# Kernel optimization log

Hardware: AMD Instinct MI355X
Metric: run time of the kernel (lower is better)

The kernel has to match this reference:

```python
import jax, jax.numpy as jnp
import numpy as np

B, S, D = 2, 4096, 2048
H = 16
DN, DR = 128, 64          # qk_nope_head_dim, qk_rope_head_dim
DQK = DN + DR             # 192
DV = 128                  # v_head_dim
QL, KVL = 512, 512        # q_lora_rank, kv_lora_rank
L = 64                    # block_len
SCALE = DQK ** -0.5
ROPE_THETA = 10000.0


def rms_norm(x, w, eps=1e-6):
    x = x.astype(jnp.float32)
    return x * jax.lax.rsqrt(jnp.mean(x * x, axis=-1, keepdims=True) + eps) * w


def apply_rope(x, cos, sin):
    # x: [b, s, h, d]; cos/sin: [s, d//2]; pairs are consecutive (view(-1,2))
    shp = x.shape
    x2 = x.reshape(shp[:-1] + (-1, 2))
    xr, xi = x2[..., 0], x2[..., 1]
    c = cos[None, :, None, :]
    s_ = sin[None, :, None, :]
    yr = xr * c - xi * s_
    yi = xr * s_ + xi * c
    return jnp.stack([yr, yi], axis=-1).reshape(shp)


def ssa(q, k, v, init_state):
    # chunked causal linear attention; q,k: [b,s,h,dk], v: [b,s,h,dv]
    b, s, h, dk = q.shape
    dv = v.shape[-1]
    nc = s // L
    qc = q.reshape(b, nc, L, h, dk)
    kc = k.reshape(b, nc, L, h, dk)
    vc = v.reshape(b, nc, L, h, dv)
    # per-chunk k^T v outer products -> [b,c,h,dk,dv]
    kv = jnp.einsum('bclhk,bclhv->bchkv', kc, vc)
    cs = jnp.cumsum(kv, axis=1)
    # exclusive prefix (state at chunk start) + initial state
    states = jnp.concatenate([jnp.zeros_like(cs[:, :1]), cs[:, :-1]], axis=1) + init_state[:, None]
    inter = jnp.einsum('bclhk,bchkv->bclhv', qc, states)
    sc = jnp.einsum('bclhk,bcmhk->bchlm', qc, kc)
    mask = jnp.tril(jnp.ones((L, L), dtype=bool))
    sc = jnp.where(mask, sc, 0.0)
    intra = jnp.einsum('bchlm,bcmhv->bclhv', sc, vc)
    return (inter + intra).reshape(b, s, h, dv)


def setup_inputs() -> dict:
    key = jax.random.key(0)
    ks = jax.random.split(key, 8)
    x = jax.random.normal(ks[0], (B, S, D), dtype=jnp.float32)
    # rope tables for qk_rope_head_dim
    inv = 1.0 / (ROPE_THETA ** (np.arange(0, DR, 2, dtype=np.float32) / DR))
    ang = np.outer(np.arange(S, dtype=np.float32), inv)
    cos = jnp.asarray(np.cos(ang), dtype=jnp.float32)
    sin = jnp.asarray(np.sin(ang), dtype=jnp.float32)
    std = 0.02
    wq_a = jax.random.normal(ks[1], (QL, D), dtype=jnp.float32) * std
    wq_b = jax.random.normal(ks[2], (H * DQK, QL), dtype=jnp.float32) * std
    wkv_a = jax.random.normal(ks[3], (KVL + DR, D), dtype=jnp.float32) * std
    wkv_b = jax.random.normal(ks[4], (H * (DN + DV), KVL), dtype=jnp.float32) * std
    wo = jax.random.normal(ks[5], (D, H * DV), dtype=jnp.float32) * std
    q_norm_w = jnp.ones((QL,), dtype=jnp.float32)
    kv_norm_w = jnp.ones((KVL,), dtype=jnp.float32)
    init_state = jnp.zeros((B, H, DQK, DV), dtype=jnp.float32)
    return {"x": x, "start_pos": 0, "cos": cos, "sin": sin,
            "wq_a": wq_a, "wq_b": wq_b, "wkv_a": wkv_a, "wkv_b": wkv_b,
            "wo": wo, "q_norm_w": q_norm_w, "kv_norm_w": kv_norm_w,
            "init_state": init_state}


def reference(x, start_pos, cos, sin, wq_a, wq_b, wkv_a, wkv_b, wo,
              q_norm_w, kv_norm_w, init_state):
    b, s, _ = x.shape
    q = rms_norm(x @ wq_a.T, q_norm_w) @ wq_b.T
    q = q.reshape(b, s, H, DQK)
    q_nope, q_pe = q[..., :DN], q[..., DN:]
    q_pe = apply_rope(q_pe, cos, sin)
    kvp = x @ wkv_a.T
    kv_lat, k_pe = kvp[..., :KVL], kvp[..., KVL:]
    k_pe = apply_rope(k_pe[:, :, None, :], cos, sin)  # [b,s,1,DR]
    kv = rms_norm(kv_lat, kv_norm_w) @ wkv_b.T
    kv = kv.reshape(b, s, H, DN + DV)
    k_nope, v = kv[..., :DN], kv[..., DN:]
    q = jnp.concatenate([q_nope, q_pe], axis=-1)
    k = jnp.concatenate([k_nope, jnp.broadcast_to(k_pe, (b, s, H, DR))], axis=-1)
    q = jax.nn.elu(q) + 1.0
    k = jax.nn.elu(k) + 1.0
    out = ssa(q, k, v, init_state) * SCALE
    out = out.reshape(b, s, H * DV) @ wo.T
    return out
```

## Files before the change

### kernel.cpp

```cpp
#include <hip/hip_runtime.h>

static __device__ __align__(256) unsigned char g_ws[645200000];

typedef __attribute__((ext_vector_type(8))) __bf16 bf16x8;
typedef __attribute__((ext_vector_type(4))) float  f32x4;
typedef __attribute__((ext_vector_type(8))) unsigned short u16x8;

__device__ __forceinline__ short f2bf(float f) {
    union { float f; unsigned u; } v; v.f = f;
    unsigned r = v.u + 0x7FFFu + ((v.u >> 16) & 1u);
    return (short)(r >> 16);
}
__device__ __forceinline__ float bf2f(unsigned short u) {
    union { unsigned u; float f; } v; v.u = ((unsigned)u) << 16;
    return v.f;
}
__device__ __forceinline__ float elu1(float x) {
    return x > 0.f ? x + 1.f : __expf(x);
}
__device__ __forceinline__ void gload_lds16(const void* g, void* l) {
    __builtin_amdgcn_global_load_lds(
        (const __attribute__((address_space(1))) unsigned int*)g,
        (__attribute__((address_space(3))) unsigned int*)l, 16, 0, 0);
}

#define MFMA16(a, b, c) __builtin_amdgcn_mfma_f32_16x16x32_bf16((a), (b), (c), 0, 0, 0)

__global__ __launch_bounds__(256) void cvt_bf16(
    const float* __restrict__ src, short* __restrict__ dst, int n)
{
    const int i = (blockIdx.x * 256 + threadIdx.x) * 4;
    if (i < n) {
        const float4 v = *(const float4*)(src + i);
        ushort4 o;
        o.x = (unsigned short)f2bf(v.x);
        o.y = (unsigned short)f2bf(v.y);
        o.z = (unsigned short)f2bf(v.z);
        o.w = (unsigned short)f2bf(v.w);
        *(ushort4*)(dst + i) = o;
    }
}

template <int OUT_BF16>
__global__ __launch_bounds__(512, 2) void gemm256(
    const short* __restrict__ A, int lda,
    const short* __restrict__ Bt, int ldb,
    void* __restrict__ Cv, int ldc,
    int Nvalid, int K, int nbx)
{
    __shared__ short lds[65536];
    char* ldsB = (char*)lds;
    const int t = threadIdx.x;
    const int lane = t & 63, w = t >> 6;

    const int cpx = gridDim.x >> 3;
    const int id = (blockIdx.x & 7) * cpx + (blockIdx.x >> 3);
    const int row0 = (id % nbx) * 256;
    const int col0 = (id / nbx) * 256;

    const int r_in = lane >> 2;
    const int sw_src = ((lane & 3) << 4) ^ (((lane >> 4) & 3) << 4);
    const char* aSrc = (const char*)A + ((size_t)(row0 + w * 32 + r_in) * lda) * 2 + sw_src;
    const char* bSrc = (const char*)Bt + ((size_t)(col0 + w * 32 + r_in) * ldb) * 2 + sw_src;
    const size_t aStep = (size_t)lda * 32;
    const size_t bStep = (size_t)ldb * 32;
    char* aDst = ldsB + (w * 2) * 1024 + lane * 16;
    char* bDst = ldsB + 65536 + (w * 2) * 1024 + lane * 16;

    const int wr = (w >> 2) * 128, wc = (w & 3) * 64;
    const int l15 = lane & 15;
    const int kxor = ((lane >> 4) * 16) ^ (((l15 >> 2) & 3) << 4);

    const int NT = K >> 5;

    auto STAGE = [&](int j) {
        const int sb = (j & 3) * 16384;
        const size_t kb = (size_t)j * 64;
        gload_lds16(aSrc + kb,         aDst + sb);
        gload_lds16(aSrc + kb + aStep, aDst + sb + 1024);
        gload_lds16(bSrc + kb,         bDst + sb);
        gload_lds16(bSrc + kb + bStep, bDst + sb + 1024);
    };

    f32x4 acc[8][4];
#pragma unroll
    for (int i = 0; i < 8; ++i)
#pragma unroll
        for (int j = 0; j < 4; ++j) acc[i][j] = (f32x4){0.f, 0.f, 0.f, 0.f};

    STAGE(0); STAGE(1); STAGE(2);

#pragma unroll 1
    for (int kt = 0; kt < NT; ++kt) {
        if (kt < NT - 2)        asm volatile("s_waitcnt vmcnt(8)" ::: "memory");
        else if (kt == NT - 2)  asm volatile("s_waitcnt vmcnt(4)" ::: "memory");
        else                    asm volatile("s_waitcnt vmcnt(0)" ::: "memory");
        __builtin_amdgcn_s_barrier();
        __builtin_amdgcn_sched_barrier(0);
        if (kt + 3 < NT) STAGE(kt + 3);
        const char* aS = ldsB + (kt & 3) * 16384;
        const char* bS = ldsB + 65536 + (kt & 3) * 16384;
        bf16x8 af[8], bf4[4];
#pragma unroll
        for (int i = 0; i < 8; ++i)
            af[i] = *(const bf16x8*)(aS + (wr + i * 16 + l15) * 64 + kxor);
#pragma unroll
        for (int j = 0; j < 4; ++j)
            bf4[j] = *(const bf16x8*)(bS + (wc + j * 16 + l15) * 64 + kxor);
        __builtin_amdgcn_s_setprio(1);
#pragma unroll
        for (int i = 0; i < 8; ++i)
#pragma unroll
            for (int j = 0; j < 4; ++j)
                acc[i][j] = MFMA16(af[i], bf4[j], acc[i][j]);
        __builtin_amdgcn_s_setprio(0);
    }

    const int rbase = (lane >> 4) * 4;
#pragma unroll
    for (int i = 0; i < 8; ++i)
#pragma unroll
        for (int j = 0; j < 4; ++j) {
            const int cc = col0 + wc + j * 16 + l15;
            if (cc < Nvalid) {
#pragma unroll
                for (int q = 0; q < 4; ++q) {
                    const size_t o = (size_t)(row0 + wr + i * 16 + rbase + q) * ldc + cc;
                    if (OUT_BF16) ((short*)Cv)[o] = f2bf(acc[i][j][q]);
                    else          ((float*)Cv)[o] = acc[i][j][q];
                }
            }
        }
}

__global__ __launch_bounds__(256) void rms_rope(
    const short* __restrict__ Y1,
    const float* __restrict__ qw, const float* __restrict__ kvw,
    const float* __restrict__ cosT, const float* __restrict__ sinT,
    short* __restrict__ qn, short* __restrict__ kvn, float* __restrict__ kpe)
{
    __shared__ float red[256];
    const int row = blockIdx.x;
    const int s = row & 4095;
    const int t = threadIdx.x;
    const unsigned short* yr = (const unsigned short*)(Y1 + (size_t)row * 1088);

    float v0 = bf2f(yr[t]), v1 = bf2f(yr[t + 256]);
    red[t] = v0 * v0 + v1 * v1;
    __syncthreads();
    for (int off = 128; off > 0; off >>= 1) {
        if (t < off) red[t] += red[t + off];
        __syncthreads();
    }
    float rs = rsqrtf(red[0] / 512.f + 1e-6f);
    __syncthreads();
    qn[(size_t)row * 512 + t]       = f2bf(v0 * rs * qw[t]);
    qn[(size_t)row * 512 + t + 256] = f2bf(v1 * rs * qw[t + 256]);

    float u0 = bf2f(yr[512 + t]), u1 = bf2f(yr[768 + t]);
    red[t] = u0 * u0 + u1 * u1;
    __syncthreads();
    for (int off = 128; off > 0; off >>= 1) {
        if (t < off) red[t] += red[t + off];
        __syncthreads();
    }
    float rs2 = rsqrtf(red[0] / 512.f + 1e-6f);
    kvn[(size_t)row * 512 + t]       = f2bf(u0 * rs2 * kvw[t]);
    kvn[(size_t)row * 512 + t + 256] = f2bf(u1 * rs2 * kvw[t + 256]);

    if (t < 32) {
        float xr = bf2f(yr[1024 + 2 * t]), xi = bf2f(yr[1024 + 2 * t + 1]);
        float cc = cosT[(size_t)s * 32 + t], sn = sinT[(size_t)s * 32 + t];
        kpe[(size_t)row * 64 + 2 * t]     = xr * cc - xi * sn;
        kpe[(size_t)row * 64 + 2 * t + 1] = xr * sn + xi * cc;
    }
}

__global__ __launch_bounds__(192) void build_q(
    const short* __restrict__ qbig,
    const float* __restrict__ cosT, const float* __restrict__ sinT,
    short* __restrict__ q_ssa)
{
    const int row = blockIdx.x;
    const int s = row & 4095;
    const int b = row >> 12;
    const int d = threadIdx.x;
    const unsigned short* qr = (const unsigned short*)(qbig + (size_t)row * 3072);
#pragma unroll 1
    for (int h = 0; h < 16; ++h) {
        float val;
        if (d < 128) {
            val = bf2f(qr[h * 192 + d]);
        } else {
            const int p = (d - 128) >> 1;
            const float xr = bf2f(qr[h * 192 + 128 + 2 * p]);
            const float xi = bf2f(qr[h * 192 + 128 + 2 * p + 1]);
            const float cc = cosT[(size_t)s * 32 + p];
            const float sn = sinT[(size_t)s * 32 + p];
            val = ((d & 1) == 0) ? (xr * cc - xi * sn) : (xr * sn + xi * cc);
        }
        val = elu1(val);
        q_ssa[((size_t)(b * 16 + h) * 4096 + s) * 192 + d] = f2bf(val);
    }
}

__global__ __launch_bounds__(256) void build_kv(
    const short* __restrict__ kvbig, const float* __restrict__ kpe,
    short* __restrict__ k_ssa, short* __restrict__ v_ssa)
{
    const int row = blockIdx.x;
    const int s = row & 4095;
    const int b = row >> 12;
    const int t = threadIdx.x;
    const unsigned short* kr = (const unsigned short*)(kvbig + (size_t)row * 4096);
    const float* pe = kpe + (size_t)row * 64;
#pragma unroll 1
    for (int h = 0; h < 16; ++h) {
        const size_t kbase = ((size_t)(b * 16 + h) * 4096 + s) * 192;
        const size_t vbase = ((size_t)(b * 16 + h) * 4096 + s) * 128;
        if (t < 128) {
            k_ssa[kbase + t] = f2bf(elu1(bf2f(kr[h * 256 + t])));
            v_ssa[vbase + t] = (short)kr[h * 256 + 128 + t];
        } else if (t < 192) {
            const int d = t - 128;
            k_ssa[kbase + 128 + d] = f2bf(elu1(pe[d]));
        }
    }
}

__global__ __launch_bounds__(256) void init_t_kern(
    const float* __restrict__ init, float* __restrict__ initT)
{
    __shared__ float tile[32][33];
    const int bh = blockIdx.y;
    const int tk = blockIdx.x % 6, tv = blockIdx.x / 6;
    const int r0 = threadIdx.x >> 5, c = threadIdx.x & 31;
    const float* src = init + (size_t)bh * 24576;
    float* dst = initT + (size_t)bh * 24576;
#pragma unroll
    for (int p = 0; p < 4; ++p) {
        const int rr = r0 + 8 * p;
        tile[rr][c] = src[(size_t)(tk * 32 + rr) * 128 + tv * 32 + c];
    }
    __syncthreads();
#pragma unroll
    for (int p = 0; p < 4; ++p) {
        const int rr = r0 + 8 * p;
        dst[(size_t)(tv * 32 + rr) * 192 + tk * 32 + c] = tile[c][rr];
    }
}

__global__ __launch_bounds__(256, 3) void ssa_kv(
    const short* __restrict__ k_ssa, const short* __restrict__ v_ssa,
    short* __restrict__ kvcT)
{
    __shared__ short smem[25600];
    short (*lkt)[72] = (short(*)[72])smem;
    short (*lvt)[72] = (short(*)[72])(smem + 192 * 72);
    short (*outT)[200] = (short(*)[200])smem;
    const int c = blockIdx.x, h = blockIdx.y, b = blockIdx.z;
    const int bh = b * 16 + h;
    const short* Kc = k_ssa + ((size_t)bh * 4096 + c * 64) * 192;
    const short* Vc = v_ssa + ((size_t)bh * 4096 + c * 64) * 128;
    const int t = threadIdx.x, lane = t & 63, w = t >> 6;
    const int l15 = lane & 15, kg = (lane >> 4) * 8, rbase = (lane >> 4) * 4;

    for (int i = t; i < 64 * 48; i += 256) {
        const int row = i / 48, c4 = (i % 48) * 4;
        ushort4 kv4 = *(const ushort4*)(Kc + (size_t)row * 192 + c4);
        lkt[c4 + 0][row] = (short)kv4.x;
        lkt[c4 + 1][row] = (short)kv4.y;
        lkt[c4 + 2][row] = (short)kv4.z;
        lkt[c4 + 3][row] = (short)kv4.w;
    }
    for (int i = t; i < 64 * 32; i += 256) {
        const int row = i >> 5, c4 = (i & 31) * 4;
        ushort4 vv = *(const ushort4*)(Vc + (size_t)row * 128 + c4);
        lvt[c4 + 0][row] = (short)vv.x;
        lvt[c4 + 1][row] = (short)vv.y;
        lvt[c4 + 2][row] = (short)vv.z;
        lvt[c4 + 3][row] = (short)vv.w;
    }
    __syncthreads();

    f32x4 acc[2][12];
#pragma unroll
    for (int i = 0; i < 2; ++i)
#pragma unroll
        for (int j = 0; j < 12; ++j) acc[i][j] = (f32x4){0.f, 0.f, 0.f, 0.f};
#pragma unroll
    for (int ks = 0; ks < 2; ++ks) {
        bf16x8 af[2];
#pragma unroll
        for (int i = 0; i < 2; ++i) af[i] = *(const bf16x8*)&lvt[w * 32 + i * 16 + l15][ks * 32 + kg];
#pragma unroll
        for (int j = 0; j < 12; ++j) {
            const bf16x8 bk = *(const bf16x8*)&lkt[j * 16 + l15][ks * 32 + kg];
#pragma unroll
            for (int i = 0; i < 2; ++i) acc[i][j] = MFMA16(af[i], bk, acc[i][j]);
        }
    }
    __syncthreads();
#pragma unroll
    for (int i = 0; i < 2; ++i)
#pragma unroll
        for (int j = 0; j < 12; ++j)
#pragma unroll
            for (int q = 0; q < 4; ++q)
                outT[w * 32 + i * 16 + rbase + q][j * 16 + l15] = f2bf(acc[i][j][q]);
    __syncthreads();

    short* kvp = kvcT + ((size_t)bh * 64 + c) * 24576;
    for (int i = t; i < 3072; i += 256) {
        const int s8 = i * 8;
        const int row = s8 / 192, col = s8 % 192;
        *(u16x8*)(kvp + s8) = *(const u16x8*)&outT[row][col];
    }
}

__global__ __launch_bounds__(256) void ssa_scan(
    short* __restrict__ kvc, const float* __restrict__ initT)
{
    const int bh = blockIdx.y;
    const int e8 = (blockIdx.x * 256 + threadIdx.x) * 8;
    float st[8];
    {
        const float4 i0 = *(const float4*)(initT + (size_t)bh * 24576 + e8);
        const float4 i1 = *(const float4*)(initT + (size_t)bh * 24576 + e8 + 4);
        st[0] = i0.x; st[1] = i0.y; st[2] = i0.z; st[3] = i0.w;
        st[4] = i1.x; st[5] = i1.y; st[6] = i1.z; st[7] = i1.w;
    }
    short* p = kvc + (size_t)bh * 64 * 24576 + e8;
    for (int cc = 0; cc < 64; ++cc) {
        const u16x8 v = *(const u16x8*)p;
        u16x8 o;
#pragma unroll
        for (int j = 0; j < 8; ++j) o[j] = (unsigned short)f2bf(st[j]);
        *(u16x8*)p = o;
#pragma unroll
        for (int j = 0; j < 8; ++j) st[j] += bf2f(v[j]);
        p += 24576;
    }
}

__global__ __launch_bounds__(256, 2) void ssa_out(
    const short* __restrict__ q_ssa, const short* __restrict__ k_ssa,
    const short* __restrict__ v_ssa, const short* __restrict__ states,
    short* __restrict__ attnb)
{
    __shared__ short lk[64][200];
    __shared__ short lvt[128][72];
    __shared__ short lst[128][104];
    __shared__ short lsc[64][72];
    const int c = blockIdx.x, h = blockIdx.y, b = blockIdx.z;
    const int bh = b * 16 + h;
    const short* Qb = q_ssa + ((size_t)bh * 4096 + c * 64) * 192;
    const short* Kc = k_ssa + ((size_t)bh * 4096 + c * 64) * 192;
    const short* Vc = v_ssa + ((size_t)bh * 4096 + c * 64) * 128;
    const short* st = states + ((size_t)bh * 64 + c) * 24576;
    const int t = threadIdx.x, lane = t & 63, w = t >> 6;
    const int l15 = lane & 15, kg = (lane >> 4) * 8, rbase = (lane >> 4) * 4;

    bf16x8 aq[6];
    {
        const short* Qr = Qb + (size_t)(w * 16 + l15) * 192 + kg;
#pragma unroll
        for (int ks = 0; ks < 6; ++ks) aq[ks] = *(const bf16x8*)(Qr + ks * 32);
    }
    for (int i = t; i < 1536; i += 256) {
        const int row = i / 24, c8 = (i % 24) * 8;
        *(u16x8*)&lk[row][c8] = *(const u16x8*)(Kc + (size_t)row * 192 + c8);
    }
    for (int i = t; i < 2048; i += 256) {
        const int row = i >> 5, c4 = (i & 31) * 4;
        ushort4 vv = *(const ushort4*)(Vc + (size_t)row * 128 + c4);
        lvt[c4 + 0][row] = (short)vv.x;
        lvt[c4 + 1][row] = (short)vv.y;
        lvt[c4 + 2][row] = (short)vv.z;
        lvt[c4 + 3][row] = (short)vv.w;
    }
    for (int i = t; i < 1536; i += 256) {
        const int row = i / 12, c8 = (i % 12) * 8;
        *(u16x8*)&lst[row][c8] = *(const u16x8*)(st + (size_t)row * 192 + c8);
    }
    __syncthreads();

    {
        f32x4 sc[4];
#pragma unroll
        for (int j = 0; j < 4; ++j) sc[j] = (f32x4){0.f, 0.f, 0.f, 0.f};
#pragma unroll
        for (int ks = 0; ks < 6; ++ks)
#pragma unroll
            for (int j = 0; j < 4; ++j) {
                const bf16x8 bk = *(const bf16x8*)&lk[j * 16 + l15][ks * 32 + kg];
                sc[j] = MFMA16(aq[ks], bk, sc[j]);
            }
#pragma unroll
        for (int j = 0; j < 4; ++j)
#pragma unroll
            for (int q = 0; q < 4; ++q) {
                const int l = w * 16 + rbase + q;
                const int m = j * 16 + l15;
                lsc[l][m] = f2bf((m <= l) ? sc[j][q] : 0.f);
            }
    }
    __syncthreads();

    f32x4 acc[8];
#pragma unroll
    for (int j = 0; j < 8; ++j) acc[j] = (f32x4){0.f, 0.f, 0.f, 0.f};
#pragma unroll
    for (int ks = 0; ks < 2; ++ks) {
        const bf16x8 as = *(const bf16x8*)&lsc[w * 16 + l15][ks * 32 + kg];
#pragma unroll
        for (int j = 0; j < 8; ++j) {
            const bf16x8 bv = *(const bf16x8*)&lvt[j * 16 + l15][ks * 32 + kg];
            acc[j] = MFMA16(as, bv, acc[j]);
        }
    }
#pragma unroll
    for (int ks = 0; ks < 3; ++ks)
#pragma unroll
        for (int j = 0; j < 8; ++j) {
            const bf16x8 bs = *(const bf16x8*)&lst[j * 16 + l15][ks * 32 + kg];
            acc[j] = MFMA16(aq[ks], bs, acc[j]);
        }
    __syncthreads();
    for (int i = t; i < 1536; i += 256) {
        const int row = i / 12, c8 = (i % 12) * 8;
        *(u16x8*)&lst[row][c8] = *(const u16x8*)(st + (size_t)row * 192 + 96 + c8);
    }
    __syncthreads();
#pragma unroll
    for (int ks = 3; ks < 6; ++ks)
#pragma unroll
        for (int j = 0; j < 8; ++j) {
            const bf16x8 bs = *(const bf16x8*)&lst[j * 16 + l15][(ks - 3) * 32 + kg];
            acc[j] = MFMA16(aq[ks], bs, acc[j]);
        }

    const float scale = 0.07216878364870322f;
#pragma unroll
    for (int j = 0; j < 8; ++j)
#pragma unroll
        for (int q = 0; q < 4; ++q) {
            const int l = w * 16 + rbase + q;
            const int dv = j * 16 + l15;
            attnb[((size_t)(b * 4096 + c * 64 + l)) * 2048 + h * 128 + dv] = f2bf(acc[j][q] * scale);
        }
}

extern "C" void kernel_launch(void* const* d_in, const int* in_sizes, int n_in,
                              void* d_out, int out_size, void* d_ws, size_t ws_size,
                              hipStream_t stream) {
    const float* x     = (const float*)d_in[0];
    const float* cosT  = (const float*)d_in[2];
    const float* sinT  = (const float*)d_in[3];
    const float* wq_a  = (const float*)d_in[4];
    const float* wq_b  = (const float*)d_in[5];
    const float* wkv_a = (const float*)d_in[6];
    const float* wkv_b = (const float*)d_in[7];
    const float* wo    = (const float*)d_in[8];
    const float* qw    = (const float*)d_in[9];
    const float* kvw   = (const float*)d_in[10];
    const float* init  = (const float*)d_in[11];
    float* out = (float*)d_out;

    void* base = nullptr;
    hipGetSymbolAddress(&base, HIP_SYMBOL(g_ws));
    char* ws = (char*)base;
    size_t off = 0;
    auto take = [&](size_t bytes) -> char* {
        char* p = ws + off;
        off += (bytes + 255) & ~(size_t)255;
        return p;
    };
    short* xb    = (short*)take((size_t)8192 * 2048 * 2);
    short* wab   = (short*)take((size_t)1280 * 2048 * 2);
    short* wqbb  = (short*)take((size_t)3072 * 512 * 2);
    short* wkvbb = (short*)take((size_t)4096 * 512 * 2);
    short* wob   = (short*)take((size_t)2048 * 2048 * 2);
    short* y1b   = (short*)take((size_t)8192 * 1088 * 2);
    short* qnb   = (short*)take((size_t)8192 * 512 * 2);
    short* kvnb  = (short*)take((size_t)8192 * 512 * 2);
    float* kpe   = (float*)take((size_t)8192 * 64 * 4);
    short* qbig  = (short*)take((size_t)8192 * 3072 * 2);
    short* kvbig = (short*)take((size_t)8192 * 4096 * 2);
    short* qs    = (short*)take((size_t)2 * 16 * 4096 * 192 * 2);
    short* ksb   = (short*)take((size_t)2 * 16 * 4096 * 192 * 2);
    short* vsb   = (short*)take((size_t)2 * 16 * 4096 * 128 * 2);
    short* kvcT  = (short*)take((size_t)2048 * 24576 * 2);
    float* initT = (float*)take((size_t)32 * 24576 * 4);
    short* attnb = (short*)take((size_t)8192 * 2048 * 2);

    cvt_bf16<<<(8192 * 2048 / 4 + 255) / 256, 256, 0, stream>>>(x, xb, 8192 * 2048);
    cvt_bf16<<<(512 * 2048 / 4 + 255) / 256, 256, 0, stream>>>(wq_a, wab, 512 * 2048);
    cvt_bf16<<<(576 * 2048 / 4 + 255) / 256, 256, 0, stream>>>(wkv_a, wab + (size_t)512 * 2048, 576 * 2048);
    hipMemsetAsync(wab + (size_t)1088 * 2048, 0, (size_t)192 * 2048 * 2, stream);
    cvt_bf16<<<(3072 * 512 / 4 + 255) / 256, 256, 0, stream>>>(wq_b, wqbb, 3072 * 512);
    cvt_bf16<<<(4096 * 512 / 4 + 255) / 256, 256, 0, stream>>>(wkv_b, wkvbb, 4096 * 512);
    cvt_bf16<<<(2048 * 2048 / 4 + 255) / 256, 256, 0, stream>>>(wo, wob, 2048 * 2048);
    init_t_kern<<<dim3(24, 32), 256, 0, stream>>>(init, initT);

    gemm256<1><<<160, 512, 0, stream>>>(xb, 2048, wab, 2048, y1b, 1088, 1088, 2048, 32);
    rms_rope<<<8192, 256, 0, stream>>>(y1b, qw, kvw, cosT, sinT, qnb, kvnb, kpe);
    gemm256<1><<<384, 512, 0, stream>>>(qnb, 512, wqbb, 512, qbig, 3072, 3072, 512, 32);
    build_q<<<8192, 192, 0, stream>>>(qbig, cosT, sinT, qs);
    gemm256<1><<<512, 512, 0, stream>>>(kvnb, 512, wkvbb, 512, kvbig, 4096, 4096, 512, 32);
    build_kv<<<8192, 256, 0, stream>>>(kvbig, kpe, ksb, vsb);
    ssa_kv<<<dim3(64, 16, 2), 256, 0, stream>>>(ksb, vsb, kvcT);
    ssa_scan<<<dim3(12, 32), 256, 0, stream>>>(kvcT, initT);
    ssa_out<<<dim3(64, 16, 2), 256, 0, stream>>>(qs, ksb, vsb, kvcT, attnb);
    gemm256<0><<<256, 512, 0, stream>>>(attnb, 2048, wob, 2048, out, 2048, 2048, 2048, 32);
}
```

Baseline: 641.0 us.

## Fuse RoPE/ELU/head scatter into GEMM epilogues and switch GEMM to K=64 double buffering

Removes the build_q and build_kv kernels by moving RoPE, ELU and the per-head layout scatter into the q and kv up-projection GEMM epilogues. This eliminates the qbig/kvbig intermediate round trips through HBM. The k_pe RoPE+ELU now happens in rms_rope in bf16, and a small build_kpe kernel broadcasts it across heads. Separately, the GEMM main loop changes from a 4-stage K=32 pipeline to a 2-stage K=64 pipeline with a new XOR swizzle and an extra barrier per iteration. The trade-off is a scattered-store epilogue and possibly less latency hiding in the GEMM.

```diff
diff --git a/kernel.cpp b/kernel.cpp
--- a/kernel.cpp
+++ b/kernel.cpp
@@ -41,15 +41,15 @@
     }
 }
 
-template <int OUT_BF16>
+template <int EPI>
 __global__ __launch_bounds__(512, 2) void gemm256(
     const short* __restrict__ A, int lda,
     const short* __restrict__ Bt, int ldb,
-    void* __restrict__ Cv, int ldc,
-    int Nvalid, int K, int nbx)
-{
-    __shared__ short lds[65536];
-    char* ldsB = (char*)lds;
+    void* __restrict__ C0, void* __restrict__ C1, int ldc,
+    int Nvalid, int K, int nbx,
+    const float* __restrict__ cosT, const float* __restrict__ sinT)
+{
+    __shared__ char ldsB[131072];
     const int t = threadIdx.x;
     const int lane = t & 63, w = t >> 6;
 
@@ -58,28 +58,30 @@
     const int row0 = (id % nbx) * 256;
     const int col0 = (id / nbx) * 256;
 
-    const int r_in = lane >> 2;
-    const int sw_src = ((lane & 3) << 4) ^ (((lane >> 4) & 3) << 4);
-    const char* aSrc = (const char*)A + ((size_t)(row0 + w * 32 + r_in) * lda) * 2 + sw_src;
-    const char* bSrc = (const char*)Bt + ((size_t)(col0 + w * 32 + r_in) * ldb) * 2 + sw_src;
-    const size_t aStep = (size_t)lda * 32;
-    const size_t bStep = (size_t)ldb * 32;
-    char* aDst = ldsB + (w * 2) * 1024 + lane * 16;
-    char* bDst = ldsB + 65536 + (w * 2) * 1024 + lane * 16;
+    const int r8 = lane >> 3;
+    const int srcb = (((lane & 7) ^ r8) << 4);
+    const char* aSrc = (const char*)A + ((size_t)(row0 + w * 32 + r8) * lda) * 2 + srcb;
+    const char* bSrc = (const char*)Bt + ((size_t)(col0 + w * 32 + r8) * ldb) * 2 + srcb;
+    const size_t aRow8 = (size_t)lda * 16;
+    const size_t bRow8 = (size_t)ldb * 16;
+    char* aDst = ldsB + w * 4096 + lane * 16;
+    char* bDst = ldsB + 65536 + w * 4096 + lane * 16;
 
     const int wr = (w >> 2) * 128, wc = (w & 3) * 64;
     const int l15 = lane & 15;
-    const int kxor = ((lane >> 4) * 16) ^ (((l15 >> 2) & 3) << 4);
-
-    const int NT = K >> 5;
+    const int g16 = (lane >> 4) * 16;
+    const int rxor = (l15 & 7) << 4;
+
+    const int NT = K >> 6;
 
     auto STAGE = [&](int j) {
-        const int sb = (j & 3) * 16384;
-        const size_t kb = (size_t)j * 64;
-        gload_lds16(aSrc + kb,         aDst + sb);
-        gload_lds16(aSrc + kb + aStep, aDst + sb + 1024);
-        gload_lds16(bSrc + kb,         bDst + sb);
-        gload_lds16(bSrc + kb + bStep, bDst + sb + 1024);
+        const int sb = (j & 1) * 32768;
+        const size_t kb = (size_t)j * 128;
+#pragma unroll
+        for (int p = 0; p < 4; ++p) {
+            gload_lds16(aSrc + kb + p * aRow8, aDst + sb + p * 1024);
+            gload_lds16(bSrc + kb + p * bRow8, bDst + sb + p * 1024);
+        }
     };
 
     f32x4 acc[8][4];
@@ -88,25 +90,25 @@
 #pragma unroll
         for (int j = 0; j < 4; ++j) acc[i][j] = (f32x4){0.f, 0.f, 0.f, 0.f};
 
-    STAGE(0); STAGE(1); STAGE(2);
+    STAGE(0); STAGE(1);
 
 #pragma unroll 1
     for (int kt = 0; kt < NT; ++kt) {
-        if (kt < NT - 2)        asm volatile("s_waitcnt vmcnt(8)" ::: "memory");
-        else if (kt == NT - 2)  asm volatile("s_waitcnt vmcnt(4)" ::: "memory");
-        else                    asm volatile("s_waitcnt vmcnt(0)" ::: "memory");
+        if (kt + 1 < NT) asm volatile("s_waitcnt vmcnt(8)" ::: "memory");
+        else             asm volatile("s_waitcnt vmcnt(0)" ::: "memory");
         __builtin_amdgcn_s_barrier();
         __builtin_amdgcn_sched_barrier(0);
-        if (kt + 3 < NT) STAGE(kt + 3);
-        const char* aS = ldsB + (kt & 3) * 16384;
-        const char* bS = ldsB + 65536 + (kt & 3) * 16384;
+        const char* aS = ldsB + (kt & 1) * 32768;
+        const char* bS = ldsB + 65536 + (kt & 1) * 32768;
         bf16x8 af[8], bf4[4];
 #pragma unroll
         for (int i = 0; i < 8; ++i)
-            af[i] = *(const bf16x8*)(aS + (wr + i * 16 + l15) * 64 + kxor);
+            af[i] = *(const bf16x8*)(aS + (wr + i * 16 + l15) * 128 + (g16 ^ rxor));
 #pragma unroll
         for (int j = 0; j < 4; ++j)
-            bf4[j] = *(const bf16x8*)(bS + (wc + j * 16 + l15) * 64 + kxor);
+            bf4[j] = *(const bf16x8*)(bS + (wc + j * 16 + l15) * 128 + (g16 ^ rxor));
+        asm volatile("s_waitcnt lgkmcnt(0)" ::: "memory");
+        __builtin_amdgcn_sched_barrier(0);
         __builtin_amdgcn_s_setprio(1);
 #pragma unroll
         for (int i = 0; i < 8; ++i)
@@ -114,6 +116,23 @@
             for (int j = 0; j < 4; ++j)
                 acc[i][j] = MFMA16(af[i], bf4[j], acc[i][j]);
         __builtin_amdgcn_s_setprio(0);
+#pragma unroll
+        for (int i = 0; i < 8; ++i)
+            af[i] = *(const bf16x8*)(aS + (wr + i * 16 + l15) * 128 + ((64 + g16) ^ rxor));
+#pragma unroll
+        for (int j = 0; j < 4; ++j)
+            bf4[j] = *(const bf16x8*)(bS + (wc + j * 16 + l15) * 128 + ((64 + g16) ^ rxor));
+        asm volatile("s_waitcnt lgkmcnt(0)" ::: "memory");
+        __builtin_amdgcn_sched_barrier(0);
+        __builtin_amdgcn_s_barrier();
+        if (kt + 2 < NT) STAGE(kt + 2);
+        __builtin_amdgcn_s_setprio(1);
+#pragma unroll
+        for (int i = 0; i < 8; ++i)
+#pragma unroll
+            for (int j = 0; j < 4; ++j)
+                acc[i][j] = MFMA16(af[i], bf4[j], acc[i][j]);
+        __builtin_amdgcn_s_setprio(0);
     }
 
     const int rbase = (lane >> 4) * 4;
@@ -122,12 +141,43 @@
 #pragma unroll
         for (int j = 0; j < 4; ++j) {
             const int cc = col0 + wc + j * 16 + l15;
-            if (cc < Nvalid) {
+            if (EPI <= 1) {
+                if (cc < Nvalid) {
+#pragma unroll
+                    for (int q = 0; q < 4; ++q) {
+                        const size_t o = (size_t)(row0 + wr + i * 16 + rbase + q) * ldc + cc;
+                        if (EPI == 1) ((short*)C0)[o] = f2bf(acc[i][j][q]);
+                        else          ((float*)C0)[o] = acc[i][j][q];
+                    }
+                }
+            } else if (EPI == 2) {
+                const int hh = cc / 192, d = cc - hh * 192;
 #pragma unroll
                 for (int q = 0; q < 4; ++q) {
-                    const size_t o = (size_t)(row0 + wr + i * 16 + rbase + q) * ldc + cc;
-                    if (OUT_BF16) ((short*)Cv)[o] = f2bf(acc[i][j][q]);
-                    else          ((float*)Cv)[o] = acc[i][j][q];
+                    const int row = row0 + wr + i * 16 + rbase + q;
+                    const int s = row & 4095, b = row >> 12;
+                    const float v = acc[i][j][q];
+                    const float pv = __shfl_xor(v, 1, 64);
+                    float val;
+                    if (d >= 128) {
+                        const int p = (d - 128) >> 1;
+                        const float c = cosT[(size_t)s * 32 + p];
+                        const float si = sinT[(size_t)s * 32 + p];
+                        val = ((d & 1) == 0) ? (v * c - pv * si) : (pv * si + v * c);
+                    } else val = v;
+                    ((short*)C0)[((size_t)(b * 16 + hh) * 4096 + s) * 192 + d] = f2bf(elu1(val));
+                }
+            } else {
+                const int hh = cc >> 8, d = cc & 255;
+#pragma unroll
+                for (int q = 0; q < 4; ++q) {
+                    const int row = row0 + wr + i * 16 + rbase + q;
+                    const int s = row & 4095, b = row >> 12;
+                    const float v = acc[i][j][q];
+                    if (d < 128)
+                        ((short*)C0)[((size_t)(b * 16 + hh) * 4096 + s) * 192 + d] = f2bf(elu1(v));
+                    else
+                        ((short*)C1)[((size_t)(b * 16 + hh) * 4096 + s) * 128 + d - 128] = f2bf(v);
                 }
             }
         }
@@ -137,7 +187,7 @@
     const short* __restrict__ Y1,
     const float* __restrict__ qw, const float* __restrict__ kvw,
     const float* __restrict__ cosT, const float* __restrict__ sinT,
-    short* __restrict__ qn, short* __restrict__ kvn, float* __restrict__ kpe)
+    short* __restrict__ qn, short* __restrict__ kvn, short* __restrict__ kpe)
 {
     __shared__ float red[256];
     const int row = blockIdx.x;
@@ -171,60 +221,23 @@
     if (t < 32) {
         float xr = bf2f(yr[1024 + 2 * t]), xi = bf2f(yr[1024 + 2 * t + 1]);
         float cc = cosT[(size_t)s * 32 + t], sn = sinT[(size_t)s * 32 + t];
-        kpe[(size_t)row * 64 + 2 * t]     = xr * cc - xi * sn;
-        kpe[(size_t)row * 64 + 2 * t + 1] = xr * sn + xi * cc;
-    }
-}
-
-__global__ __launch_bounds__(192) void build_q(
-    const short* __restrict__ qbig,
-    const float* __restrict__ cosT, const float* __restrict__ sinT,
-    short* __restrict__ q_ssa)
+        kpe[(size_t)row * 64 + 2 * t]     = f2bf(elu1(xr * cc - xi * sn));
+        kpe[(size_t)row * 64 + 2 * t + 1] = f2bf(elu1(xr * sn + xi * cc));
+    }
+}
+
+__global__ __launch_bounds__(256) void build_kpe(
+    const short* __restrict__ kpe, short* __restrict__ k_ssa)
 {
     const int row = blockIdx.x;
-    const int s = row & 4095;
-    const int b = row >> 12;
-    const int d = threadIdx.x;
-    const unsigned short* qr = (const unsigned short*)(qbig + (size_t)row * 3072);
-#pragma unroll 1
-    for (int h = 0; h < 16; ++h) {
-        float val;
-        if (d < 128) {
-            val = bf2f(qr[h * 192 + d]);
-        } else {
-            const int p = (d - 128) >> 1;
-            const float xr = bf2f(qr[h * 192 + 128 + 2 * p]);
-            const float xi = bf2f(qr[h * 192 + 128 + 2 * p + 1]);
-            const float cc = cosT[(size_t)s * 32 + p];
-            const float sn = sinT[(size_t)s * 32 + p];
-            val = ((d & 1) == 0) ? (xr * cc - xi * sn) : (xr * sn + xi * cc);
-        }
-        val = elu1(val);
-        q_ssa[((size_t)(b * 16 + h) * 4096 + s) * 192 + d] = f2bf(val);
-    }
-}
-
-__global__ __launch_bounds__(256) void build_kv(
-    const short* __restrict__ kvbig, const float* __restrict__ kpe,
-    short* __restrict__ k_ssa, short* __restrict__ v_ssa)
-{
-    const int row = blockIdx.x;
-    const int s = row & 4095;
-    const int b = row >> 12;
+    const int s = row & 4095, b = row >> 12;
     const int t = threadIdx.x;
-    const unsigned short* kr = (const unsigned short*)(kvbig + (size_t)row * 4096);
-    const float* pe = kpe + (size_t)row * 64;
-#pragma unroll 1
-    for (int h = 0; h < 16; ++h) {
-        const size_t kbase = ((size_t)(b * 16 + h) * 4096 + s) * 192;
-        const size_t vbase = ((size_t)(b * 16 + h) * 4096 + s) * 128;
-        if (t < 128) {
-            k_ssa[kbase + t] = f2bf(elu1(bf2f(kr[h * 256 + t])));
-            v_ssa[vbase + t] = (short)kr[h * 256 + 128 + t];
-        } else if (t < 192) {
-            const int d = t - 128;
-            k_ssa[kbase + 128 + d] = f2bf(elu1(pe[d]));
-        }
+    const short* pe = kpe + (size_t)row * 64;
+#pragma unroll
+    for (int it = 0; it < 4; ++it) {
+        const int idx = t + it * 256;
+        const int h = idx >> 6, dd = idx & 63;
+        k_ssa[((size_t)(b * 16 + h) * 4096 + s) * 192 + 128 + dd] = pe[dd];
     }
 }
 
@@ -484,9 +497,7 @@
     short* y1b   = (short*)take((size_t)8192 * 1088 * 2);
     short* qnb   = (short*)take((size_t)8192 * 512 * 2);
     short* kvnb  = (short*)take((size_t)8192 * 512 * 2);
-    float* kpe   = (float*)take((size_t)8192 * 64 * 4);
-    short* qbig  = (short*)take((size_t)8192 * 3072 * 2);
-    short* kvbig = (short*)take((size_t)8192 * 4096 * 2);
+    short* kpe   = (short*)take((size_t)8192 * 64 * 2);
     short* qs    = (short*)take((size_t)2 * 16 * 4096 * 192 * 2);
     short* ksb   = (short*)take((size_t)2 * 16 * 4096 * 192 * 2);
     short* vsb   = (short*)take((size_t)2 * 16 * 4096 * 128 * 2);
@@ -503,14 +514,13 @@
     cvt_bf16<<<(2048 * 2048 / 4 + 255) / 256, 256, 0, stream>>>(wo, wob, 2048 * 2048);
     init_t_kern<<<dim3(24, 32), 256, 0, stream>>>(init, initT);
 
-    gemm256<1><<<160, 512, 0, stream>>>(xb, 2048, wab, 2048, y1b, 1088, 1088, 2048, 32);
+    gemm256<1><<<160, 512, 0, stream>>>(xb, 2048, wab, 2048, y1b, nullptr, 1088, 1088, 2048, 32, nullptr, nullptr);
     rms_rope<<<8192, 256, 0, stream>>>(y1b, qw, kvw, cosT, sinT, qnb, kvnb, kpe);
-    gemm256<1><<<384, 512, 0, stream>>>(qnb, 512, wqbb, 512, qbig, 3072, 3072, 512, 32);
-    build_q<<<8192, 192, 0, stream>>>(qbig, cosT, sinT, qs);
-    gemm256<1><<<512, 512, 0, stream>>>(kvnb, 512, wkvbb, 512, kvbig, 4096, 4096, 512, 32);
-    build_kv<<<8192, 256, 0, stream>>>(kvbig, kpe, ksb, vsb);
+    gemm256<2><<<384, 512, 0, stream>>>(qnb, 512, wqbb, 512, qs, nullptr, 0, 3072, 512, 32, cosT, sinT);
+    gemm256<3><<<512, 512, 0, stream>>>(kvnb, 512, wkvbb, 512, ksb, vsb, 0, 4096, 512, 32, nullptr, nullptr);
+    build_kpe<<<8192, 256, 0, stream>>>(kpe, ksb);
     ssa_kv<<<dim3(64, 16, 2), 256, 0, stream>>>(ksb, vsb, kvcT);
     ssa_scan<<<dim3(12, 32), 256, 0, stream>>>(kvcT, initT);
     ssa_out<<<dim3(64, 16, 2), 256, 0, stream>>>(qs, ksb, vsb, kvcT, attnb);
-    gemm256<0><<<256, 512, 0, stream>>>(attnb, 2048, wob, 2048, out, 2048, 2048, 2048, 32);
-}
+    gemm256<0><<<256, 512, 0, stream>>>(attnb, 2048, wob, 2048, out, nullptr, 2048, 2048, 2048, 32, nullptr, nullptr);
+}
```

New measurement: 623.2 us. 2.8% less time.
